# Kernel optimization log

Measured on AMD Instinct MI355X. Metric: run time of the kernel, lower is better.

The kernel has to match this reference:

```python
import jax, jax.numpy as jnp
import numpy as np

B, N, H, NH = 8, 1024, 512, 8
DK = H // NH


def setup_inputs() -> dict:
    key = jax.random.key(0)
    ks = jax.random.split(key, 6)
    x = jax.random.normal(ks[0], (B, N, H), dtype=jnp.float32)
    adj = jax.random.randint(ks[1], (B, N, N), 0, 2, dtype=jnp.int32)
    # ensure no all-zero row (self-loops) so softmax is well-defined
    adj = jnp.maximum(adj, jnp.eye(N, dtype=jnp.int32)[None])
    s = 1.0 / np.sqrt(H)
    Wq = jax.random.normal(ks[2], (H, H), dtype=jnp.float32) * s
    Wk = jax.random.normal(ks[3], (H, H), dtype=jnp.float32) * s
    Wv = jax.random.normal(ks[4], (H, H), dtype=jnp.float32) * s
    Wg = jax.random.normal(ks[5], (H, 2 * H), dtype=jnp.float32) * (1.0 / np.sqrt(2 * H))
    bg = jnp.zeros((H,), dtype=jnp.float32)
    return {"x": x, "adj": adj, "Wq": Wq, "Wk": Wk, "Wv": Wv, "Wg": Wg, "bg": bg}


def reference(x, adj, Wq, Wk, Wv, Wg, bg):
    b, n, h = x.shape
    # projections (nn.Linear: x @ W.T), split heads -> [b, n, nh, dk]
    q = (x @ Wq.T).reshape(b, n, NH, DK)
    k = (x @ Wk.T).reshape(b, n, NH, DK)
    v = (x @ Wv.T).reshape(b, n, NH, DK)
    # scaled masked attention: [b, nh, n, n]
    scores = jnp.einsum('bqhd,bkhd->bhqk', q, k) / jnp.sqrt(jnp.float32(DK))
    mask = (adj != 0)[:, None, :, :]
    scores = jnp.where(mask, scores, -jnp.inf)
    attn = jax.nn.softmax(scores, axis=-1)  # dropout p=0.0 -> identity
    c = jnp.einsum('bhqk,bkhd->bqhd', attn, v).reshape(b, n, h)
    # sigmoid gated residual combine
    gate = jax.nn.sigmoid(jnp.concatenate([c, x], axis=2) @ Wg.T + bg)
    return gate * x + (1.0 - gate) * c
```

## Files before the change

kernel.cpp:

```cpp
#include <hip/hip_runtime.h>
#include <math.h>

#define B_  8
#define N_  1024
#define H_  512
#define NH_ 8
#define DK_ 64
#define M_  (B_ * N_)

typedef __attribute__((ext_vector_type(4))) float f32x4;
typedef __attribute__((ext_vector_type(8))) short bf16x8;

__device__ __forceinline__ unsigned short f2bf(float f) {
    unsigned int u = __float_as_uint(f);
    u = (u + 0x7fffu + ((u >> 16) & 1u)) >> 16;
    return (unsigned short)u;
}

__device__ __forceinline__ void gload16(const unsigned short* g, unsigned short* l) {
    __builtin_amdgcn_global_load_lds(
        (const __attribute__((address_space(1))) void*)g,
        (__attribute__((address_space(3))) void*)l, 16, 0, 0);
}

__global__ __launch_bounds__(256) void cvt_k(const float* __restrict__ src,
                                             unsigned short* __restrict__ dst, int n)
{
    int i = (blockIdx.x * 256 + threadIdx.x) * 4;
    if (i < n) {
        float4 v = *(const float4*)&src[i];
        *(ushort4*)&dst[i] = make_ushort4(f2bf(v.x), f2bf(v.y), f2bf(v.z), f2bf(v.w));
    }
}

__global__ __launch_bounds__(256) void pack_k(const int* __restrict__ adj,
                                              unsigned long long* __restrict__ mb)
{
    int gw   = (int)((blockIdx.x * 256 + threadIdx.x) >> 6);
    int lane = threadIdx.x & 63;
    int kt = gw & 15;
    int q  = (gw >> 4) & (N_ - 1);
    int b  = gw >> 14;
    int val = adj[(size_t)(b * N_ + q) * N_ + kt * 64 + lane];
    unsigned long long m = __ballot(val != 0);
    if (lane == 0) mb[gw] = m;
}

__global__ __launch_bounds__(256, 2) void proj_k(const unsigned short* __restrict__ xb,
                                                 const unsigned short* __restrict__ Wqb,
                                                 const unsigned short* __restrict__ Wkb,
                                                 const unsigned short* __restrict__ Wvb,
                                                 unsigned short* __restrict__ qkv)
{
    __shared__ unsigned short As[8192];
    __shared__ unsigned short Bs[8192];
    const int tid = threadIdx.x;
    const int lane = tid & 63, wv = tid >> 6;
    const int ln = lane & 15, quad = lane >> 4;
    const int wm = wv >> 1, wn = wv & 1;
    const int row0 = blockIdx.x * 128;
    const int w    = blockIdx.y >> 2;
    const int col0 = (blockIdx.y & 3) * 128;
    const unsigned short* W = (w == 0) ? Wqb : ((w == 1) ? Wkb : Wvb);
    f32x4 acc[4][4] = {};

    for (int kt = 0; kt < H_; kt += 64) {
        __syncthreads();
        #pragma unroll
        for (int i = 0; i < 4; ++i) {
            int c = tid + i * 256;
            int c8 = c >> 7, row = c & 127;
            gload16(&xb[(size_t)(row0 + row) * H_ + kt + c8 * 8], &As[c * 8]);
            gload16(&W [(size_t)(col0 + row) * H_ + kt + c8 * 8], &Bs[c * 8]);
        }
        __syncthreads();
        #pragma unroll
        for (int kk = 0; kk < 2; ++kk) {
            bf16x8 af[4], bf[4];
            #pragma unroll
            for (int t = 0; t < 4; ++t) {
                af[t] = *(const bf16x8*)&As[((kk * 4 + quad) * 128 + wm * 64 + t * 16 + ln) * 8];
                bf[t] = *(const bf16x8*)&Bs[((kk * 4 + quad) * 128 + wn * 64 + t * 16 + ln) * 8];
            }
            #pragma unroll
            for (int mt = 0; mt < 4; ++mt)
                #pragma unroll
                for (int nt = 0; nt < 4; ++nt)
                    acc[mt][nt] = __builtin_amdgcn_mfma_f32_16x16x32_bf16(af[mt], bf[nt], acc[mt][nt], 0, 0, 0);
        }
    }
    #pragma unroll
    for (int mt = 0; mt < 4; ++mt)
        #pragma unroll
        for (int nt = 0; nt < 4; ++nt)
            #pragma unroll
            for (int r = 0; r < 4; ++r) {
                int m = row0 + wm * 64 + mt * 16 + quad * 4 + r;
                int c = w * H_ + col0 + wn * 64 + nt * 16 + ln;
                qkv[(size_t)m * (3 * H_) + c] = f2bf(acc[mt][nt][r]);
            }
}

__global__ __launch_bounds__(256) void transp_k(const unsigned short* __restrict__ qkv,
                                                unsigned short* __restrict__ Vt)
{
    __shared__ unsigned short Ts[64][72];
    const int bh = blockIdx.x;
    const int n0 = blockIdx.y * 64;
    const int b = bh >> 3, h = bh & 7;
    const int tid = threadIdx.x;
    #pragma unroll
    for (int p = 0; p < 2; ++p) {
        int row = (tid >> 3) + p * 32;
        int ch  = tid & 7;
        *(uint4*)&Ts[row][ch * 8] =
            *(const uint4*)&qkv[(size_t)(b * N_ + n0 + row) * (3 * H_) + 2 * H_ + h * DK_ + ch * 8];
    }
    __syncthreads();
    #pragma unroll
    for (int p = 0; p < 16; ++p) {
        int d = (tid >> 6) + p * 4;
        int n = tid & 63;
        Vt[((size_t)bh * DK_ + d) * N_ + n0 + n] = Ts[n][d];
    }
}

__global__ __launch_bounds__(256, 4) void attn_k(const unsigned short* __restrict__ qkv,
                                                 const unsigned short* __restrict__ Vt,
                                                 const unsigned long long* __restrict__ Mb,
                                                 unsigned short* __restrict__ Cmb)
{
    const int nqt  = N_ / 64;
    const int qt   = blockIdx.x % nqt;
    const int head = (blockIdx.x / nqt) % NH_;
    const int b    = blockIdx.x / (nqt * NH_);

    __shared__ unsigned short Ks[4096];
    __shared__ unsigned short Vs[4096];
    __shared__ unsigned short Ps[4][16][72];

    const int tid = threadIdx.x;
    const int lane = tid & 63, wv = tid >> 6;
    const int ln = lane & 15, quad = lane >> 4;
    const int q = qt * 64 + wv * 16 + ln;

    bf16x8 bq[2];
    #pragma unroll
    for (int kk = 0; kk < 2; ++kk)
        bq[kk] = *(const bf16x8*)&qkv[(size_t)(b * N_ + q) * (3 * H_) + head * DK_ + kk * 32 + quad * 8];

    f32x4 o[4] = {};
    float psum = 0.f;
    const unsigned short* Kbase = qkv + H_ + head * DK_;

    for (int t = 0; t < 16; ++t) {
        const int kc = t * 64;
        __syncthreads();
        #pragma unroll
        for (int i = 0; i < 2; ++i) {
            int c = tid + i * 256;
            int c8 = c >> 6, row = c & 63;
            gload16(&Kbase[(size_t)(b * N_ + kc + row) * (3 * H_) + c8 * 8], &Ks[c * 8]);
            gload16(&Vt[((size_t)(b * NH_ + head) * DK_ + row) * N_ + kc + c8 * 8], &Vs[c * 8]);
        }
        __syncthreads();

        unsigned long long mq = Mb[(size_t)(b * N_ + q) * 16 + t];

        f32x4 s[4] = {};
        #pragma unroll
        for (int kk = 0; kk < 2; ++kk)
            #pragma unroll
            for (int nt = 0; nt < 4; ++nt) {
                bf16x8 ka = *(const bf16x8*)&Ks[((kk * 4 + quad) * 64 + nt * 16 + ln) * 8];
                s[nt] = __builtin_amdgcn_mfma_f32_16x16x32_bf16(ka, bq[kk], s[nt], 0, 0, 0);
            }

        unsigned long long sh = mq >> (quad * 4);
        #pragma unroll
        for (int nt = 0; nt < 4; ++nt) {
            unsigned int bn = (unsigned int)(sh >> (nt * 16)) & 0xFu;
            float p[4];
            #pragma unroll
            for (int r = 0; r < 4; ++r) {
                float e = __expf(s[nt][r] * 0.125f);
                p[r] = (bn & (1u << r)) ? e : 0.f;
                psum += p[r];
            }
            unsigned int d0 = __builtin_amdgcn_perm(__float_as_uint(p[1]), __float_as_uint(p[0]), 0x07060302u);
            unsigned int d1 = __builtin_amdgcn_perm(__float_as_uint(p[3]), __float_as_uint(p[2]), 0x07060302u);
            *(uint2*)&Ps[wv][ln][nt * 16 + quad * 4] = make_uint2(d0, d1);
        }

        bf16x8 pb[2];
        #pragma unroll
        for (int kk = 0; kk < 2; ++kk)
            pb[kk] = *(const bf16x8*)&Ps[wv][ln][kk * 32 + quad * 8];
        #pragma unroll
        for (int kk = 0; kk < 2; ++kk)
            #pragma unroll
            for (int dt = 0; dt < 4; ++dt) {
                bf16x8 va = *(const bf16x8*)&Vs[((kk * 4 + quad) * 64 + dt * 16 + ln) * 8];
                o[dt] = __builtin_amdgcn_mfma_f32_16x16x32_bf16(va, pb[kk], o[dt], 0, 0, 0);
            }
    }

    psum += __shfl_xor(psum, 16);
    psum += __shfl_xor(psum, 32);
    float inv = 1.f / psum;

    #pragma unroll
    for (int dt = 0; dt < 4; ++dt) {
        ushort4 u = make_ushort4(f2bf(o[dt][0] * inv), f2bf(o[dt][1] * inv),
                                 f2bf(o[dt][2] * inv), f2bf(o[dt][3] * inv));
        *(ushort4*)&Cmb[(size_t)(b * N_ + q) * H_ + head * DK_ + dt * 16 + quad * 4] = u;
    }
}

__global__ __launch_bounds__(256, 2) void gate_k(const unsigned short* __restrict__ cmb,
                                                 const unsigned short* __restrict__ xb,
                                                 const unsigned short* __restrict__ Wgb,
                                                 const float* __restrict__ bgp,
                                                 const float* __restrict__ X,
                                                 float* __restrict__ out)
{
    __shared__ unsigned short As[8192];
    __shared__ unsigned short Bs[4096];
    const int tid = threadIdx.x;
    const int lane = tid & 63, wv = tid >> 6;
    const int ln = lane & 15, quad = lane >> 4;
    const int wm = wv >> 1, wn = wv & 1;
    const int row0 = blockIdx.x * 128;
    const int col0 = blockIdx.y * 64;
    f32x4 acc[4][2] = {};

    for (int kt = 0; kt < 2 * H_; kt += 64) {
        const unsigned short* Asrc = (kt < H_) ? cmb : xb;
        const int ko = kt & (H_ - 1);
        __syncthreads();
        #pragma unroll
        for (int i = 0; i < 4; ++i) {
            int c = tid + i * 256;
            int c8 = c >> 7, row = c & 127;
            gload16(&Asrc[(size_t)(row0 + row) * H_ + ko + c8 * 8], &As[c * 8]);
        }
        #pragma unroll
        for (int i = 0; i < 2; ++i) {
            int c = tid + i * 256;
            int c8 = c >> 6, row = c & 63;
            gload16(&Wgb[(size_t)(col0 + row) * (2 * H_) + kt + c8 * 8], &Bs[c * 8]);
        }
        __syncthreads();
        #pragma unroll
        for (int kk = 0; kk < 2; ++kk) {
            bf16x8 af[4], bf[2];
            #pragma unroll
            for (int t = 0; t < 4; ++t)
                af[t] = *(const bf16x8*)&As[((kk * 4 + quad) * 128 + wm * 64 + t * 16 + ln) * 8];
            #pragma unroll
            for (int t = 0; t < 2; ++t)
                bf[t] = *(const bf16x8*)&Bs[((kk * 4 + quad) * 64 + wn * 32 + t * 16 + ln) * 8];
            #pragma unroll
            for (int mt = 0; mt < 4; ++mt)
                #pragma unroll
                for (int nt = 0; nt < 2; ++nt)
                    acc[mt][nt] = __builtin_amdgcn_mfma_f32_16x16x32_bf16(af[mt], bf[nt], acc[mt][nt], 0, 0, 0);
        }
    }
    #pragma unroll
    for (int mt = 0; mt < 4; ++mt)
        #pragma unroll
        for (int nt = 0; nt < 2; ++nt)
            #pragma unroll
            for (int r = 0; r < 4; ++r) {
                int m = row0 + wm * 64 + mt * 16 + quad * 4 + r;
                int c = col0 + wn * 32 + nt * 16 + ln;
                float g  = 1.f / (1.f + __expf(-(acc[mt][nt][r] + bgp[c])));
                float xv = X[(size_t)m * H_ + c];
                float cv = __uint_as_float(((unsigned int)cmb[(size_t)m * H_ + c]) << 16);
                out[(size_t)m * H_ + c] = g * xv + (1.f - g) * cv;
            }
}

extern "C" void kernel_launch(void* const* d_in, const int* in_sizes, int n_in,
                              void* d_out, int out_size, void* d_ws, size_t ws_size,
                              hipStream_t stream)
{
    const float* x   = (const float*)d_in[0];
    const int*   adj = (const int*)  d_in[1];
    const float* Wq  = (const float*)d_in[2];
    const float* Wk  = (const float*)d_in[3];
    const float* Wv  = (const float*)d_in[4];
    const float* Wg  = (const float*)d_in[5];
    const float* bg  = (const float*)d_in[6];
    float* out = (float*)d_out;

    unsigned short* xb  = (unsigned short*)d_ws;
    unsigned short* wqb = xb  + (size_t)M_ * H_;
    unsigned short* wkb = wqb + (size_t)H_ * H_;
    unsigned short* wvb = wkb + (size_t)H_ * H_;
    unsigned short* wgb = wvb + (size_t)H_ * H_;
    unsigned short* qkv = wgb + (size_t)H_ * 2 * H_;
    unsigned short* vt  = qkv + (size_t)M_ * 3 * H_;
    unsigned short* cmb = vt  + (size_t)M_ * H_;
    unsigned long long* mb = (unsigned long long*)(cmb + (size_t)M_ * H_);

    cvt_k<<<M_ * H_ / 1024, 256, 0, stream>>>(x, xb, M_ * H_);
    cvt_k<<<H_ * H_ / 1024, 256, 0, stream>>>(Wq, wqb, H_ * H_);
    cvt_k<<<H_ * H_ / 1024, 256, 0, stream>>>(Wk, wkb, H_ * H_);
    cvt_k<<<H_ * H_ / 1024, 256, 0, stream>>>(Wv, wvb, H_ * H_);
    cvt_k<<<H_ * 2 * H_ / 1024, 256, 0, stream>>>(Wg, wgb, H_ * 2 * H_);

    pack_k<<<M_ * 16 / 4, 256, 0, stream>>>(adj, mb);

    proj_k<<<dim3(M_ / 128, 12), 256, 0, stream>>>(xb, wqb, wkb, wvb, qkv);

    transp_k<<<dim3(B_ * NH_, N_ / 64), 256, 0, stream>>>(qkv, vt);

    attn_k<<<B_ * NH_ * (N_ / 64), 256, 0, stream>>>(qkv, vt, mb, cmb);

    gate_k<<<dim3(M_ / 128, H_ / 64), 256, 0, stream>>>(cmb, xb, wgb, bg, x, out);
}
```

Baseline: 234.5 us.

## Fuse prep kernels, write V transposed from projection, drop LDS staging in attention

Merges the five conversion kernels and the adjacency packing into one launch. The projection writes V directly in transposed layout, so the separate transpose kernel goes away. The attention kernel now reads K and V straight from global memory instead of staging them in LDS behind barriers. The softmax scale and log2(e) are folded into Wq so exp2 can replace expf. The gate epilogue reads the bf16 x copy instead of fp32 x, which adds rounding error to the residual term and relies on cache hits for the unstaged K/V reads.

```diff
diff --git a/kernel.cpp b/kernel.cpp
--- a/kernel.cpp
+++ b/kernel.cpp
@@ -17,40 +17,67 @@
     return (unsigned short)u;
 }
 
+__device__ __forceinline__ float bf2f(unsigned short s) {
+    return __uint_as_float(((unsigned int)s) << 16);
+}
+
+__device__ __forceinline__ float fexp2(float x) {
+#if __has_builtin(__builtin_amdgcn_exp2f)
+    return __builtin_amdgcn_exp2f(x);
+#else
+    return exp2f(x);
+#endif
+}
+
 __device__ __forceinline__ void gload16(const unsigned short* g, unsigned short* l) {
     __builtin_amdgcn_global_load_lds(
         (const __attribute__((address_space(1))) void*)g,
         (__attribute__((address_space(3))) void*)l, 16, 0, 0);
 }
 
-__global__ __launch_bounds__(256) void cvt_k(const float* __restrict__ src,
-                                             unsigned short* __restrict__ dst, int n)
-{
-    int i = (blockIdx.x * 256 + threadIdx.x) * 4;
-    if (i < n) {
-        float4 v = *(const float4*)&src[i];
-        *(ushort4*)&dst[i] = make_ushort4(f2bf(v.x), f2bf(v.y), f2bf(v.z), f2bf(v.w));
-    }
-}
-
-__global__ __launch_bounds__(256) void pack_k(const int* __restrict__ adj,
+__global__ __launch_bounds__(256) void prep_k(const float* __restrict__ x,
+                                              const float* __restrict__ Wq,
+                                              const float* __restrict__ Wk,
+                                              const float* __restrict__ Wv,
+                                              const float* __restrict__ Wg,
+                                              const int*   __restrict__ adj,
+                                              unsigned short* __restrict__ xb,
+                                              unsigned short* __restrict__ wqb,
+                                              unsigned short* __restrict__ wkb,
+                                              unsigned short* __restrict__ wvb,
+                                              unsigned short* __restrict__ wgb,
                                               unsigned long long* __restrict__ mb)
 {
-    int gw   = (int)((blockIdx.x * 256 + threadIdx.x) >> 6);
-    int lane = threadIdx.x & 63;
-    int kt = gw & 15;
-    int q  = (gw >> 4) & (N_ - 1);
-    int b  = gw >> 14;
-    int val = adj[(size_t)(b * N_ + q) * N_ + kt * 64 + lane];
-    unsigned long long m = __ballot(val != 0);
-    if (lane == 0) mb[gw] = m;
-}
-
-__global__ __launch_bounds__(256, 2) void proj_k(const unsigned short* __restrict__ xb,
+    int id = blockIdx.x;
+    if (id >= 5376) {
+        int gw   = (id - 5376) * 4 + (threadIdx.x >> 6);
+        int lane = threadIdx.x & 63;
+        int kt = gw & 15;
+        int q  = (gw >> 4) & (N_ - 1);
+        int b  = gw >> 14;
+        int val = adj[(size_t)(b * N_ + q) * N_ + kt * 64 + lane];
+        unsigned long long m = __ballot(val != 0);
+        if (lane == 0) mb[gw] = m;
+        return;
+    }
+    const float* src; unsigned short* dst; int off; float scale = 1.0f;
+    if (id < 4096)      { src = x;  dst = xb;  off = id; }
+    else if (id < 4352) { src = Wq; dst = wqb; off = id - 4096; scale = 0.18033688011112042f; }
+    else if (id < 4608) { src = Wk; dst = wkb; off = id - 4352; }
+    else if (id < 4864) { src = Wv; dst = wvb; off = id - 4608; }
+    else                { src = Wg; dst = wgb; off = id - 4864; }
+    size_t i = (size_t)off * 1024 + threadIdx.x * 4;
+    float4 v = *(const float4*)&src[i];
+    *(ushort4*)&dst[i] = make_ushort4(f2bf(v.x * scale), f2bf(v.y * scale),
+                                      f2bf(v.z * scale), f2bf(v.w * scale));
+}
+
+__global__ __launch_bounds__(256, 3) void proj_k(const unsigned short* __restrict__ xb,
                                                  const unsigned short* __restrict__ Wqb,
                                                  const unsigned short* __restrict__ Wkb,
                                                  const unsigned short* __restrict__ Wvb,
-                                                 unsigned short* __restrict__ qkv)
+                                                 unsigned short* __restrict__ qk,
+                                                 unsigned short* __restrict__ vt)
 {
     __shared__ unsigned short As[8192];
     __shared__ unsigned short Bs[8192];
@@ -89,54 +116,42 @@
                     acc[mt][nt] = __builtin_amdgcn_mfma_f32_16x16x32_bf16(af[mt], bf[nt], acc[mt][nt], 0, 0, 0);
         }
     }
-    #pragma unroll
-    for (int mt = 0; mt < 4; ++mt)
-        #pragma unroll
-        for (int nt = 0; nt < 4; ++nt)
-            #pragma unroll
-            for (int r = 0; r < 4; ++r) {
-                int m = row0 + wm * 64 + mt * 16 + quad * 4 + r;
-                int c = w * H_ + col0 + wn * 64 + nt * 16 + ln;
-                qkv[(size_t)m * (3 * H_) + c] = f2bf(acc[mt][nt][r]);
-            }
-}
-
-__global__ __launch_bounds__(256) void transp_k(const unsigned short* __restrict__ qkv,
-                                                unsigned short* __restrict__ Vt)
-{
-    __shared__ unsigned short Ts[64][72];
-    const int bh = blockIdx.x;
-    const int n0 = blockIdx.y * 64;
-    const int b = bh >> 3, h = bh & 7;
-    const int tid = threadIdx.x;
-    #pragma unroll
-    for (int p = 0; p < 2; ++p) {
-        int row = (tid >> 3) + p * 32;
-        int ch  = tid & 7;
-        *(uint4*)&Ts[row][ch * 8] =
-            *(const uint4*)&qkv[(size_t)(b * N_ + n0 + row) * (3 * H_) + 2 * H_ + h * DK_ + ch * 8];
-    }
-    __syncthreads();
-    #pragma unroll
-    for (int p = 0; p < 16; ++p) {
-        int d = (tid >> 6) + p * 4;
-        int n = tid & 63;
-        Vt[((size_t)bh * DK_ + d) * N_ + n0 + n] = Ts[n][d];
-    }
-}
-
-__global__ __launch_bounds__(256, 4) void attn_k(const unsigned short* __restrict__ qkv,
+    if (w < 2) {
+        #pragma unroll
+        for (int mt = 0; mt < 4; ++mt)
+            #pragma unroll
+            for (int nt = 0; nt < 4; ++nt)
+                #pragma unroll
+                for (int r = 0; r < 4; ++r) {
+                    int m = row0 + wm * 64 + mt * 16 + quad * 4 + r;
+                    int c = w * H_ + col0 + wn * 64 + nt * 16 + ln;
+                    qk[(size_t)m * (2 * H_) + c] = f2bf(acc[mt][nt][r]);
+                }
+    } else {
+        #pragma unroll
+        for (int mt = 0; mt < 4; ++mt)
+            #pragma unroll
+            for (int nt = 0; nt < 4; ++nt) {
+                int c = col0 + wn * 64 + nt * 16 + ln;
+                int head = c >> 6, d = c & 63;
+                int m0 = row0 + wm * 64 + mt * 16 + quad * 4;
+                int bb = m0 >> 10, n = m0 & (N_ - 1);
+                ushort4 u = make_ushort4(f2bf(acc[mt][nt][0]), f2bf(acc[mt][nt][1]),
+                                         f2bf(acc[mt][nt][2]), f2bf(acc[mt][nt][3]));
+                *(ushort4*)&vt[((size_t)(bb * NH_ + head) * DK_ + d) * N_ + n] = u;
+            }
+    }
+}
+
+__global__ __launch_bounds__(256, 4) void attn_k(const unsigned short* __restrict__ qk,
                                                  const unsigned short* __restrict__ Vt,
                                                  const unsigned long long* __restrict__ Mb,
                                                  unsigned short* __restrict__ Cmb)
 {
-    const int nqt  = N_ / 64;
-    const int qt   = blockIdx.x % nqt;
-    const int head = (blockIdx.x / nqt) % NH_;
-    const int b    = blockIdx.x / (nqt * NH_);
-
-    __shared__ unsigned short Ks[4096];
-    __shared__ unsigned short Vs[4096];
+    const int qt   = blockIdx.x & 15;
+    const int head = (blockIdx.x >> 4) & 7;
+    const int b    = blockIdx.x >> 7;
+
     __shared__ unsigned short Ps[4][16][72];
 
     const int tid = threadIdx.x;
@@ -144,35 +159,28 @@
     const int ln = lane & 15, quad = lane >> 4;
     const int q = qt * 64 + wv * 16 + ln;
 
+    const unsigned short* Qrow = &qk[(size_t)(b * N_ + q) * (2 * H_) + head * DK_];
     bf16x8 bq[2];
-    #pragma unroll
-    for (int kk = 0; kk < 2; ++kk)
-        bq[kk] = *(const bf16x8*)&qkv[(size_t)(b * N_ + q) * (3 * H_) + head * DK_ + kk * 32 + quad * 8];
+    bq[0] = *(const bf16x8*)&Qrow[quad * 8];
+    bq[1] = *(const bf16x8*)&Qrow[32 + quad * 8];
+
+    const unsigned short* Kb = &qk[(size_t)(b * N_) * (2 * H_) + H_ + head * DK_];
+    const unsigned short* Vb = &Vt[(size_t)(b * NH_ + head) * DK_ * N_];
+    const unsigned long long* mrow = &Mb[(size_t)(b * N_ + q) * 16];
 
     f32x4 o[4] = {};
     float psum = 0.f;
-    const unsigned short* Kbase = qkv + H_ + head * DK_;
 
     for (int t = 0; t < 16; ++t) {
         const int kc = t * 64;
-        __syncthreads();
-        #pragma unroll
-        for (int i = 0; i < 2; ++i) {
-            int c = tid + i * 256;
-            int c8 = c >> 6, row = c & 63;
-            gload16(&Kbase[(size_t)(b * N_ + kc + row) * (3 * H_) + c8 * 8], &Ks[c * 8]);
-            gload16(&Vt[((size_t)(b * NH_ + head) * DK_ + row) * N_ + kc + c8 * 8], &Vs[c * 8]);
-        }
-        __syncthreads();
-
-        unsigned long long mq = Mb[(size_t)(b * N_ + q) * 16 + t];
+        unsigned long long mq = mrow[t];
 
         f32x4 s[4] = {};
         #pragma unroll
         for (int kk = 0; kk < 2; ++kk)
             #pragma unroll
             for (int nt = 0; nt < 4; ++nt) {
-                bf16x8 ka = *(const bf16x8*)&Ks[((kk * 4 + quad) * 64 + nt * 16 + ln) * 8];
+                bf16x8 ka = *(const bf16x8*)&Kb[(size_t)(kc + nt * 16 + ln) * (2 * H_) + kk * 32 + quad * 8];
                 s[nt] = __builtin_amdgcn_mfma_f32_16x16x32_bf16(ka, bq[kk], s[nt], 0, 0, 0);
             }
 
@@ -183,7 +191,7 @@
             float p[4];
             #pragma unroll
             for (int r = 0; r < 4; ++r) {
-                float e = __expf(s[nt][r] * 0.125f);
+                float e = fexp2(s[nt][r]);
                 p[r] = (bn & (1u << r)) ? e : 0.f;
                 psum += p[r];
             }
@@ -193,14 +201,14 @@
         }
 
         bf16x8 pb[2];
+        pb[0] = *(const bf16x8*)&Ps[wv][ln][quad * 8];
+        pb[1] = *(const bf16x8*)&Ps[wv][ln][32 + quad * 8];
+
         #pragma unroll
         for (int kk = 0; kk < 2; ++kk)
-            pb[kk] = *(const bf16x8*)&Ps[wv][ln][kk * 32 + quad * 8];
-        #pragma unroll
-        for (int kk = 0; kk < 2; ++kk)
             #pragma unroll
             for (int dt = 0; dt < 4; ++dt) {
-                bf16x8 va = *(const bf16x8*)&Vs[((kk * 4 + quad) * 64 + dt * 16 + ln) * 8];
+                bf16x8 va = *(const bf16x8*)&Vb[(size_t)(dt * 16 + ln) * N_ + kc + kk * 32 + quad * 8];
                 o[dt] = __builtin_amdgcn_mfma_f32_16x16x32_bf16(va, pb[kk], o[dt], 0, 0, 0);
             }
     }
@@ -221,7 +229,6 @@
                                                  const unsigned short* __restrict__ xb,
                                                  const unsigned short* __restrict__ Wgb,
                                                  const float* __restrict__ bgp,
-                                                 const float* __restrict__ X,
                                                  float* __restrict__ out)
 {
     __shared__ unsigned short As[8192];
@@ -276,8 +283,8 @@
                 int m = row0 + wm * 64 + mt * 16 + quad * 4 + r;
                 int c = col0 + wn * 32 + nt * 16 + ln;
                 float g  = 1.f / (1.f + __expf(-(acc[mt][nt][r] + bgp[c])));
-                float xv = X[(size_t)m * H_ + c];
-                float cv = __uint_as_float(((unsigned int)cmb[(size_t)m * H_ + c]) << 16);
+                float xv = bf2f(xb[(size_t)m * H_ + c]);
+                float cv = bf2f(cmb[(size_t)m * H_ + c]);
                 out[(size_t)m * H_ + c] = g * xv + (1.f - g) * cv;
             }
 }
@@ -300,24 +307,17 @@
     unsigned short* wkb = wqb + (size_t)H_ * H_;
     unsigned short* wvb = wkb + (size_t)H_ * H_;
     unsigned short* wgb = wvb + (size_t)H_ * H_;
-    unsigned short* qkv = wgb + (size_t)H_ * 2 * H_;
-    unsigned short* vt  = qkv + (size_t)M_ * 3 * H_;
+    unsigned short* qk  = wgb + (size_t)H_ * 2 * H_;
+    unsigned short* vt  = qk  + (size_t)M_ * 2 * H_;
     unsigned short* cmb = vt  + (size_t)M_ * H_;
     unsigned long long* mb = (unsigned long long*)(cmb + (size_t)M_ * H_);
 
-    cvt_k<<<M_ * H_ / 1024, 256, 0, stream>>>(x, xb, M_ * H_);
-    cvt_k<<<H_ * H_ / 1024, 256, 0, stream>>>(Wq, wqb, H_ * H_);
-    cvt_k<<<H_ * H_ / 1024, 256, 0, stream>>>(Wk, wkb, H_ * H_);
-    cvt_k<<<H_ * H_ / 1024, 256, 0, stream>>>(Wv, wvb, H_ * H_);
-    cvt_k<<<H_ * 2 * H_ / 1024, 256, 0, stream>>>(Wg, wgb, H_ * 2 * H_);
-
-    pack_k<<<M_ * 16 / 4, 256, 0, stream>>>(adj, mb);
-
-    proj_k<<<dim3(M_ / 128, 12), 256, 0, stream>>>(xb, wqb, wkb, wvb, qkv);
-
-    transp_k<<<dim3(B_ * NH_, N_ / 64), 256, 0, stream>>>(qkv, vt);
-
-    attn_k<<<B_ * NH_ * (N_ / 64), 256, 0, stream>>>(qkv, vt, mb, cmb);
-
-    gate_k<<<dim3(M_ / 128, H_ / 64), 256, 0, stream>>>(cmb, xb, wgb, bg, x, out);
-}
+    prep_k<<<5376 + 32768, 256, 0, stream>>>(x, Wq, Wk, Wv, Wg, adj,
+                                             xb, wqb, wkb, wvb, wgb, mb);
+
+    proj_k<<<dim3(M_ / 128, 12), 256, 0, stream>>>(xb, wqb, wkb, wvb, qk, vt);
+
+    attn_k<<<B_ * NH_ * (N_ / 64), 256, 0, stream>>>(qk, vt, mb, cmb);
+
+    gate_k<<<dim3(M_ / 128, H_ / 64), 256, 0, stream>>>(cmb, xb, wgb, bg, out);
+}
```

New measurement: 290.4 us. +23.8%, slower.
